# Performance work log

Hardware: AMD Instinct MI355X
Metric: run time of the kernel (lower is better)

Reference implementation:

```python
import jax, jax.numpy as jnp
import numpy as np

LN_EPS = 1e-5

def setup_inputs() -> dict:
    key = jax.random.key(0)
    k0, k1, k2, k3 = jax.random.split(key, 4)
    B, N, D = 4, 4096, 512
    x = jax.random.normal(k0, (B, N, D), dtype=jnp.float32)
    s = 1.0 / np.sqrt(D)
    Wq = jax.random.normal(k1, (D, D), dtype=jnp.float32) * s
    Wk = jax.random.normal(k2, (D, D), dtype=jnp.float32) * s
    Wv = jax.random.normal(k3, (D, D), dtype=jnp.float32) * s
    gamma = jnp.ones((D,), dtype=jnp.float32)
    beta = jnp.zeros((D,), dtype=jnp.float32)
    return {"x": x, "Wq": Wq, "Wk": Wk, "Wv": Wv, "gamma": gamma, "beta": beta}

def reference(x, Wq, Wk, Wv, gamma, beta):
    # x: [B, N, D]
    D = x.shape[-1]
    q = jnp.einsum('bnd,de->bne', x, Wq)
    k = jnp.einsum('bnd,de->bne', x, Wk)
    v = jnp.einsum('bnd,de->bne', x, Wv)
    # full [B, N, N] score matrix, as in the original bmm chain
    dist = jnp.einsum('bne,bme->bnm', q, k) * (1.0 / jnp.sqrt(jnp.float32(D)))
    dist = jax.nn.softmax(dist, axis=-1)
    att = jnp.einsum('bnm,bmd->bnd', dist, v)
    # residual + LayerNorm over last dim
    h = att + x
    mu = jnp.mean(h, axis=-1, keepdims=True)
    var = jnp.mean(jnp.square(h - mu), axis=-1, keepdims=True)
    out = (h - mu) * jax.lax.rsqrt(var + LN_EPS) * gamma + beta
    return out
```

## Files before the change

### kernel.cpp

```cpp
#include <hip/hip_runtime.h>
#include <stdint.h>

typedef __attribute__((ext_vector_type(8))) __bf16 bf16x8;
typedef __attribute__((ext_vector_type(4))) float f32x4;
typedef __attribute__((ext_vector_type(16))) float f32x16;
typedef unsigned short u16;
typedef unsigned char u8;
typedef unsigned int u32;
typedef long i64;

#define LN_EPS 1e-5f

__device__ __forceinline__ float bf2f(u16 u){
  union { u32 i; float f; } v; v.i = ((u32)u) << 16; return v.f;
}
__device__ __forceinline__ u16 f2bf(float f){
  union { float f; u32 i; } v; v.f = f;
  u32 u = v.i;
  u += 0x7fffu + ((u >> 16) & 1u);
  return (u16)(u >> 16);
}
__device__ __forceinline__ u8 f2fp8(float f){
  union { float f; u32 i; } v; v.f = f;
  u32 s = (v.i >> 24) & 0x80u;
  u32 u = v.i & 0x7FFFFFFFu;
  if (u < 0x3C800000u) return (u8)s;
  if (u > 0x43E00000u) u = 0x43E00000u;
  u += 0x7FFFFu + ((u >> 20) & 1u);
  int e = (int)(u >> 23) - 120;
  u32 m = (u >> 20) & 7u;
  return (u8)(s | ((u32)e << 3) | m);
}

__device__ __forceinline__ void gload_lds16(const void* g, void* l) {
  __builtin_amdgcn_global_load_lds(
      (const __attribute__((address_space(1))) void*)g,
      (__attribute__((address_space(3))) void*)l, 16, 0, 0);
}

__global__ void transpose_w_kernel(const float* __restrict__ Wq,
                                   const float* __restrict__ Wk,
                                   const float* __restrict__ Wv,
                                   u16* __restrict__ Wt) {
  const float* W = (blockIdx.y == 0) ? Wq : ((blockIdx.y == 1) ? Wk : Wv);
  u16* o = Wt + blockIdx.y * 512 * 512;
  int idx = blockIdx.x * 256 + threadIdx.x;
  int e = idx >> 9, d = idx & 511;
  o[e * 512 + d] = f2bf(W[d * 512 + e]);
}

__launch_bounds__(256, 2)
__global__ void qkv_gemm_kernel(const float* __restrict__ X,
                                const u16* __restrict__ Wt,
                                u8* __restrict__ Qo,
                                u8* __restrict__ Ko,
                                u16* __restrict__ Vto) {
  const int z = blockIdx.y;
  const u16* Wtm = Wt + z * 512 * 512;
  const int mblk = blockIdx.x & 127;
  const int nblk = blockIdx.x >> 7;
  const int m0 = mblk * 128, n0 = nblk * 128;

  __shared__ u16 As[128 * 40];
  __shared__ u16 Bs[128 * 40];

  const int tid = threadIdx.x;
  const int lane = tid & 63, w = tid >> 6;
  const int wr = w >> 1, wc = w & 1;
  const int lrow = lane & 15, quad = lane >> 4;

  f32x4 acc[4][4];
#pragma unroll
  for (int i = 0; i < 4; i++)
#pragma unroll
    for (int j = 0; j < 4; j++) acc[i][j] = (f32x4){0.f, 0.f, 0.f, 0.f};

  for (int k0 = 0; k0 < 512; k0 += 32) {
    __syncthreads();
#pragma unroll
    for (int i = 0; i < 2; i++) {
      int c = tid + i * 256;
      int r = c >> 2, cc = (c & 3) * 8;
      float4 f0 = *(const float4*)&X[(m0 + r) * 512 + k0 + cc];
      float4 f1 = *(const float4*)&X[(m0 + r) * 512 + k0 + cc + 4];
      ushort4 lo, hi;
      lo.x = f2bf(f0.x); lo.y = f2bf(f0.y); lo.z = f2bf(f0.z); lo.w = f2bf(f0.w);
      hi.x = f2bf(f1.x); hi.y = f2bf(f1.y); hi.z = f2bf(f1.z); hi.w = f2bf(f1.w);
      *(ushort4*)&As[r * 40 + cc] = lo;
      *(ushort4*)&As[r * 40 + cc + 4] = hi;
      uint4 vb = *(const uint4*)&Wtm[(n0 + r) * 512 + k0 + cc];
      *(uint4*)&Bs[r * 40 + cc] = vb;
    }
    __syncthreads();
    bf16x8 a[4], b[4];
#pragma unroll
    for (int t = 0; t < 4; t++)
      a[t] = *(const bf16x8*)&As[(wr * 64 + t * 16 + lrow) * 40 + quad * 8];
#pragma unroll
    for (int t = 0; t < 4; t++)
      b[t] = *(const bf16x8*)&Bs[(wc * 64 + t * 16 + lrow) * 40 + quad * 8];
#pragma unroll
    for (int i = 0; i < 4; i++)
#pragma unroll
      for (int j = 0; j < 4; j++)
        acc[i][j] = __builtin_amdgcn_mfma_f32_16x16x32_bf16(a[i], b[j], acc[i][j], 0, 0, 0);
  }

  if (z < 2) {
    u8* O = (z == 0) ? Qo : Ko;
#pragma unroll
    for (int i = 0; i < 4; i++) {
      int rbase = m0 + wr * 64 + i * 16 + quad * 4;
#pragma unroll
      for (int j = 0; j < 4; j++) {
        int col = n0 + wc * 64 + j * 16 + lrow;
#pragma unroll
        for (int r = 0; r < 4; r++)
          O[(rbase + r) * 512 + col] = f2fp8(acc[i][j][r]);
      }
    }
  } else {
#pragma unroll
    for (int i = 0; i < 4; i++) {
      int rbase = m0 + wr * 64 + i * 16 + quad * 4;
#pragma unroll
      for (int j = 0; j < 4; j++) {
        int col = n0 + wc * 64 + j * 16 + lrow;
        ushort4 pk;
        pk.x = f2bf(acc[i][j][0]);
        pk.y = f2bf(acc[i][j][1]);
        pk.z = f2bf(acc[i][j][2]);
        pk.w = f2bf(acc[i][j][3]);
        *(ushort4*)&Vto[col * 16384 + rbase] = pk;
      }
    }
  }
}

__launch_bounds__(256, 2)
__global__ void attn_partial_kernel(const u8* __restrict__ Q,
                                    const u8* __restrict__ K,
                                    const u16* __restrict__ Vt,
                                    float* __restrict__ O0,
                                    u16* __restrict__ O1,
                                    float* __restrict__ L) {
  const int b = blockIdx.y;
  const int split = blockIdx.z;
  const int q0 = blockIdx.x * 64;
  const int tid = threadIdx.x;
  const int lane = tid & 63, w = tid >> 6;
  const int lrow = lane & 15, quad = lane >> 4;
  const int l31 = lane & 31, half = lane >> 5;

  __shared__ __align__(16) u8 Ks8[32 * 512];
  __shared__ u16 Vs[512 * 32];
  __shared__ u16 Pbuf[64 * 40];

  const int keybase = b * 4096 + split * 2048;

  const int qtok = b * 4096 + q0 + w * 16 + lrow;
  i64 qf[16];
#pragma unroll
  for (int s = 0; s < 16; s++)
    qf[s] = *(const i64*)&Q[qtok * 512 + s * 32 + quad * 8];

  f32x16 Oacc[2][4];
#pragma unroll
  for (int i = 0; i < 2; i++)
#pragma unroll
    for (int j = 0; j < 4; j++)
#pragma unroll
      for (int e = 0; e < 16; e++) Oacc[i][j][e] = 0.f;

  float lsum[4] = {0.f, 0.f, 0.f, 0.f};
  const float scale = 0.044194173824159216f;

#pragma unroll
  for (int i = 0; i < 4; i++) {
    int row = w * 8 + i * 2 + (lane >> 5);
    int g = (lane & 31) ^ (row & 7);
    gload_lds16(&K[(keybase + row) * 512 + g * 16], &Ks8[(w * 8 + i * 2) * 512]);
  }
#pragma unroll
  for (int run = 0; run < 8; run++) {
    int rr = w * 8 + run;
    int n = rr * 16 + (lane >> 2);
    int c = (lane & 3) ^ (n & 3) ^ ((n >> 2) & 3);
    gload_lds16(&Vt[n * 16384 + keybase + c * 8], &Vs[rr * 512]);
  }

  for (int it = 0; it < 64; ++it) {
    __syncthreads();

    f32x4 S0 = {0.f, 0.f, 0.f, 0.f}, S1 = {0.f, 0.f, 0.f, 0.f};
#pragma unroll
    for (int s = 0; s < 16; s++) {
      int gs = (2 * s + (quad >> 1)) ^ (lrow & 7);
      int off = gs * 16 + (quad & 1) * 8;
      i64 k0 = *(const i64*)&Ks8[lrow * 512 + off];
      i64 k1 = *(const i64*)&Ks8[(16 + lrow) * 512 + off];
      S0 = __builtin_amdgcn_mfma_f32_16x16x32_fp8_fp8(qf[s], k0, S0, 0, 0, 0);
      S1 = __builtin_amdgcn_mfma_f32_16x16x32_fp8_fp8(qf[s], k1, S1, 0, 0, 0);
    }

#pragma unroll
    for (int r = 0; r < 4; r++) {
      float p0 = __expf(S0[r] * scale);
      float p1 = __expf(S1[r] * scale);
      lsum[r] += p0 + p1;
      int prow = w * 16 + quad * 4 + r;
      Pbuf[prow * 40 + lrow] = f2bf(p0);
      Pbuf[prow * 40 + 16 + lrow] = f2bf(p1);
    }

    __syncthreads();

    const int kknext = (it + 1) * 32;
    if (it < 63) {
#pragma unroll
      for (int i = 0; i < 4; i++) {
        int row = w * 8 + i * 2 + (lane >> 5);
        int g = (lane & 31) ^ (row & 7);
        gload_lds16(&K[(keybase + kknext + row) * 512 + g * 16],
                    &Ks8[(w * 8 + i * 2) * 512]);
      }
    }

    bf16x8 af[2][2];
#pragma unroll
    for (int i = 0; i < 2; i++)
#pragma unroll
      for (int kg = 0; kg < 2; kg++)
        af[i][kg] = *(const bf16x8*)&Pbuf[(i * 32 + l31) * 40 + kg * 16 + half * 8];

    bf16x8 bv[4][2];
#pragma unroll
    for (int j = 0; j < 4; j++)
#pragma unroll
      for (int kg = 0; kg < 2; kg++) {
        int n = w * 128 + j * 32 + l31;
        int c = (kg * 2 + half) ^ (n & 3) ^ ((n >> 2) & 3);
        bv[j][kg] = *(const bf16x8*)&Vs[n * 32 + c * 8];
      }

    asm volatile("s_waitcnt lgkmcnt(0)" ::: "memory");

    if (it < 63) {
#pragma unroll
      for (int run = 0; run < 8; run++) {
        int rr = w * 8 + run;
        int n = rr * 16 + (lane >> 2);
        int c = (lane & 3) ^ (n & 3) ^ ((n >> 2) & 3);
        gload_lds16(&Vt[n * 16384 + keybase + kknext + c * 8], &Vs[rr * 512]);
      }
    }

#pragma unroll
    for (int j = 0; j < 4; j++)
#pragma unroll
      for (int i = 0; i < 2; i++) {
        Oacc[i][j] = __builtin_amdgcn_mfma_f32_32x32x16_bf16(af[i][0], bv[j][0], Oacc[i][j], 0, 0, 0);
        Oacc[i][j] = __builtin_amdgcn_mfma_f32_32x32x16_bf16(af[i][1], bv[j][1], Oacc[i][j], 0, 0, 0);
      }
  }

#pragma unroll
  for (int r = 0; r < 4; r++) {
    float s = lsum[r];
    s += __shfl_xor(s, 1); s += __shfl_xor(s, 2);
    s += __shfl_xor(s, 4); s += __shfl_xor(s, 8);
    lsum[r] = s;
  }
  const int tokw = b * 4096 + q0 + w * 16 + quad * 4;
  if (lrow == 0) {
#pragma unroll
    for (int r = 0; r < 4; r++)
      L[split * 16384 + tokw + r] = lsum[r];
  }

  const int tokbase = b * 4096 + q0;
  if (split == 0) {
#pragma unroll
    for (int i = 0; i < 2; i++)
#pragma unroll
      for (int j = 0; j < 4; j++) {
        int col = w * 128 + j * 32 + l31;
#pragma unroll
        for (int p = 0; p < 16; p++) {
          int row = i * 32 + (p & 3) + 8 * (p >> 2) + 4 * half;
          O0[(tokbase + row) * 512 + col] = Oacc[i][j][p];
        }
      }
  } else {
#pragma unroll
    for (int i = 0; i < 2; i++)
#pragma unroll
      for (int j = 0; j < 4; j++) {
        int col = w * 128 + j * 32 + l31;
#pragma unroll
        for (int p = 0; p < 16; p++) {
          int row = i * 32 + (p & 3) + 8 * (p >> 2) + 4 * half;
          O1[(tokbase + row) * 512 + col] = f2bf(Oacc[i][j][p]);
        }
      }
  }
}

__launch_bounds__(256)
__global__ void combine_ln_kernel(const float* __restrict__ O0in,
                                  const u16* __restrict__ O1,
                                  const float* __restrict__ L,
                                  const float* __restrict__ X,
                                  const float* __restrict__ gamma,
                                  const float* __restrict__ beta,
                                  float* __restrict__ Out) {
  const int lane = threadIdx.x & 63;
  const int tok = blockIdx.x * 4 + (threadIdx.x >> 6);
  const float inv_l = 1.f / (L[tok] + L[16384 + tok]);
  const int base = tok * 512 + lane * 8;

  float4 a0 = *(const float4*)&O0in[base];
  float4 a1 = *(const float4*)&O0in[base + 4];
  uint4 bvec = *(const uint4*)&O1[base];
  const u16* bp = (const u16*)&bvec;
  float4 x0 = *(const float4*)&X[base];
  float4 x1 = *(const float4*)&X[base + 4];

  float h[8];
  h[0] = (a0.x + bf2f(bp[0])) * inv_l + x0.x;
  h[1] = (a0.y + bf2f(bp[1])) * inv_l + x0.y;
  h[2] = (a0.z + bf2f(bp[2])) * inv_l + x0.z;
  h[3] = (a0.w + bf2f(bp[3])) * inv_l + x0.w;
  h[4] = (a1.x + bf2f(bp[4])) * inv_l + x1.x;
  h[5] = (a1.y + bf2f(bp[5])) * inv_l + x1.y;
  h[6] = (a1.z + bf2f(bp[6])) * inv_l + x1.z;
  h[7] = (a1.w + bf2f(bp[7])) * inv_l + x1.w;

  float sum = 0.f, sq = 0.f;
#pragma unroll
  for (int i = 0; i < 8; i++) { sum += h[i]; sq += h[i] * h[i]; }
#pragma unroll
  for (int d = 1; d < 64; d <<= 1) {
    sum += __shfl_xor(sum, d);
    sq  += __shfl_xor(sq, d);
  }
  float mu = sum * (1.f / 512.f);
  float var = sq * (1.f / 512.f) - mu * mu;
  float rstd = rsqrtf(var + LN_EPS);

  float4 g0 = *(const float4*)&gamma[lane * 8];
  float4 g1 = *(const float4*)&gamma[lane * 8 + 4];
  float4 b0 = *(const float4*)&beta[lane * 8];
  float4 b1 = *(const float4*)&beta[lane * 8 + 4];

  float4 o0, o1;
  o0.x = (h[0] - mu) * rstd * g0.x + b0.x;
  o0.y = (h[1] - mu) * rstd * g0.y + b0.y;
  o0.z = (h[2] - mu) * rstd * g0.z + b0.z;
  o0.w = (h[3] - mu) * rstd * g0.w + b0.w;
  o1.x = (h[4] - mu) * rstd * g1.x + b1.x;
  o1.y = (h[5] - mu) * rstd * g1.y + b1.y;
  o1.z = (h[6] - mu) * rstd * g1.z + b1.z;
  o1.w = (h[7] - mu) * rstd * g1.w + b1.w;
  *(float4*)&Out[base] = o0;
  *(float4*)&Out[base + 4] = o1;
}

extern "C" void kernel_launch(void* const* d_in, const int* in_sizes, int n_in,
                              void* d_out, int out_size, void* d_ws, size_t ws_size,
                              hipStream_t stream) {
  const float* x = (const float*)d_in[0];
  const float* Wq = (const float*)d_in[1];
  const float* Wk = (const float*)d_in[2];
  const float* Wv = (const float*)d_in[3];
  const float* gamma = (const float*)d_in[4];
  const float* beta = (const float*)d_in[5];

  char* ws = (char*)d_ws;
  u8*  Qws   = (u8*)(ws);
  u8*  Kws   = (u8*)(ws + 8388608);
  u16* Vtws  = (u16*)(ws + 16777216);
  u16* Wtws  = (u16*)(ws + 33554432);
  u16* O1ws  = (u16*)(ws + 35127296);
  float* Lws = (float*)(ws + 51904512);
  float* O0  = (float*)d_out;

  hipLaunchKernelGGL(transpose_w_kernel, dim3(1024, 3), dim3(256), 0, stream,
                     Wq, Wk, Wv, Wtws);
  hipLaunchKernelGGL(qkv_gemm_kernel, dim3(512, 3), dim3(256), 0, stream,
                     x, Wtws, Qws, Kws, Vtws);
  hipLaunchKernelGGL(attn_partial_kernel, dim3(64, 4, 2), dim3(256), 0, stream,
                     Qws, Kws, Vtws, O0, O1ws, Lws);
  hipLaunchKernelGGL(combine_ln_kernel, dim3(4096), dim3(256), 0, stream,
                     O0, O1ws, Lws, x, gamma, beta, (float*)d_out);
}
```

Measured before the change: 290.8 us.

## Switch PV to fp8 MFMA, pre-cast X to bf16, async-load GEMM tiles

The attention PV product now uses fp8 probabilities and an fp8 transposed V with 32x32x16 fp8 MFMAs, which halves V staging bytes and LDS traffic. X is cast to bf16 in a separate kernel so the QKV GEMM can load tiles straight into swizzled LDS with global_load_lds, and the GEMM now asks for higher occupancy. Both partial attention outputs are stored as bf16 rather than one in fp32, which cuts write and read traffic in the combine step. The cost is lower precision in P and V, which could hurt accuracy, plus an extra launch and a reuse of the Xb workspace as O0b.

Measured after the change: 282.9 us. 1.03x faster.

```diff
diff --git a/kernel.cpp b/kernel.cpp
--- a/kernel.cpp
+++ b/kernel.cpp
@@ -38,6 +38,17 @@
       (__attribute__((address_space(3))) void*)l, 16, 0, 0);
 }
 
+__global__ void xcast_kernel(const float* __restrict__ X, u16* __restrict__ Xb) {
+  int idx = (blockIdx.x * 256 + threadIdx.x) * 8;
+  float4 f0 = *(const float4*)&X[idx];
+  float4 f1 = *(const float4*)&X[idx + 4];
+  ushort4 lo, hi;
+  lo.x = f2bf(f0.x); lo.y = f2bf(f0.y); lo.z = f2bf(f0.z); lo.w = f2bf(f0.w);
+  hi.x = f2bf(f1.x); hi.y = f2bf(f1.y); hi.z = f2bf(f1.z); hi.w = f2bf(f1.w);
+  *(ushort4*)&Xb[idx] = lo;
+  *(ushort4*)&Xb[idx + 4] = hi;
+}
+
 __global__ void transpose_w_kernel(const float* __restrict__ Wq,
                                    const float* __restrict__ Wk,
                                    const float* __restrict__ Wv,
@@ -49,20 +60,20 @@
   o[e * 512 + d] = f2bf(W[d * 512 + e]);
 }
 
-__launch_bounds__(256, 2)
-__global__ void qkv_gemm_kernel(const float* __restrict__ X,
+__launch_bounds__(256, 4)
+__global__ void qkv_gemm_kernel(const u16* __restrict__ Xb,
                                 const u16* __restrict__ Wt,
                                 u8* __restrict__ Qo,
                                 u8* __restrict__ Ko,
-                                u16* __restrict__ Vto) {
+                                u8* __restrict__ Vto8) {
   const int z = blockIdx.y;
   const u16* Wtm = Wt + z * 512 * 512;
   const int mblk = blockIdx.x & 127;
   const int nblk = blockIdx.x >> 7;
   const int m0 = mblk * 128, n0 = nblk * 128;
 
-  __shared__ u16 As[128 * 40];
-  __shared__ u16 Bs[128 * 40];
+  __shared__ __align__(16) u8 As[128 * 64];
+  __shared__ __align__(16) u8 Bs[128 * 64];
 
   const int tid = threadIdx.x;
   const int lane = tid & 63, w = tid >> 6;
@@ -75,30 +86,40 @@
 #pragma unroll
     for (int j = 0; j < 4; j++) acc[i][j] = (f32x4){0.f, 0.f, 0.f, 0.f};
 
-  for (int k0 = 0; k0 < 512; k0 += 32) {
-    __syncthreads();
-#pragma unroll
-    for (int i = 0; i < 2; i++) {
-      int c = tid + i * 256;
-      int r = c >> 2, cc = (c & 3) * 8;
-      float4 f0 = *(const float4*)&X[(m0 + r) * 512 + k0 + cc];
-      float4 f1 = *(const float4*)&X[(m0 + r) * 512 + k0 + cc + 4];
-      ushort4 lo, hi;
-      lo.x = f2bf(f0.x); lo.y = f2bf(f0.y); lo.z = f2bf(f0.z); lo.w = f2bf(f0.w);
-      hi.x = f2bf(f1.x); hi.y = f2bf(f1.y); hi.z = f2bf(f1.z); hi.w = f2bf(f1.w);
-      *(ushort4*)&As[r * 40 + cc] = lo;
-      *(ushort4*)&As[r * 40 + cc + 4] = hi;
-      uint4 vb = *(const uint4*)&Wtm[(n0 + r) * 512 + k0 + cc];
-      *(uint4*)&Bs[r * 40 + cc] = vb;
-    }
+  const int srow = lane >> 2;
+  const int spos = lane & 3;
+
+#pragma unroll
+  for (int r2 = 0; r2 < 2; r2++) {
+    int rowb = w * 32 + r2 * 16;
+    int row = rowb + srow;
+    int g = spos ^ (row & 3);
+    gload_lds16(&Xb[(m0 + row) * 512 + g * 8], &As[rowb * 64]);
+    gload_lds16(&Wtm[(n0 + row) * 512 + g * 8], &Bs[rowb * 64]);
+  }
+
+  for (int k = 0; k < 16; k++) {
     __syncthreads();
     bf16x8 a[4], b[4];
 #pragma unroll
-    for (int t = 0; t < 4; t++)
-      a[t] = *(const bf16x8*)&As[(wr * 64 + t * 16 + lrow) * 40 + quad * 8];
-#pragma unroll
-    for (int t = 0; t < 4; t++)
-      b[t] = *(const bf16x8*)&Bs[(wc * 64 + t * 16 + lrow) * 40 + quad * 8];
+    for (int t = 0; t < 4; t++) {
+      int ra = wr * 64 + t * 16 + lrow;
+      a[t] = *(const bf16x8*)&As[ra * 64 + (quad ^ (ra & 3)) * 16];
+      int rb = wc * 64 + t * 16 + lrow;
+      b[t] = *(const bf16x8*)&Bs[rb * 64 + (quad ^ (rb & 3)) * 16];
+    }
+    __syncthreads();
+    if (k < 15) {
+      int k0n = (k + 1) * 32;
+#pragma unroll
+      for (int r2 = 0; r2 < 2; r2++) {
+        int rowb = w * 32 + r2 * 16;
+        int row = rowb + srow;
+        int g = spos ^ (row & 3);
+        gload_lds16(&Xb[(m0 + row) * 512 + k0n + g * 8], &As[rowb * 64]);
+        gload_lds16(&Wtm[(n0 + row) * 512 + k0n + g * 8], &Bs[rowb * 64]);
+      }
+    }
 #pragma unroll
     for (int i = 0; i < 4; i++)
 #pragma unroll
@@ -126,12 +147,12 @@
 #pragma unroll
       for (int j = 0; j < 4; j++) {
         int col = n0 + wc * 64 + j * 16 + lrow;
-        ushort4 pk;
-        pk.x = f2bf(acc[i][j][0]);
-        pk.y = f2bf(acc[i][j][1]);
-        pk.z = f2bf(acc[i][j][2]);
-        pk.w = f2bf(acc[i][j][3]);
-        *(ushort4*)&Vto[col * 16384 + rbase] = pk;
+        uchar4 pk;
+        pk.x = f2fp8(acc[i][j][0]);
+        pk.y = f2fp8(acc[i][j][1]);
+        pk.z = f2fp8(acc[i][j][2]);
+        pk.w = f2fp8(acc[i][j][3]);
+        *(uchar4*)&Vto8[col * 16384 + rbase] = pk;
       }
     }
   }
@@ -140,9 +161,9 @@
 __launch_bounds__(256, 2)
 __global__ void attn_partial_kernel(const u8* __restrict__ Q,
                                     const u8* __restrict__ K,
-                                    const u16* __restrict__ Vt,
-                                    float* __restrict__ O0,
-                                    u16* __restrict__ O1,
+                                    const u8* __restrict__ Vt8,
+                                    u16* __restrict__ O0b,
+                                    u16* __restrict__ O1b,
                                     float* __restrict__ L) {
   const int b = blockIdx.y;
   const int split = blockIdx.z;
@@ -153,8 +174,8 @@
   const int l31 = lane & 31, half = lane >> 5;
 
   __shared__ __align__(16) u8 Ks8[32 * 512];
-  __shared__ u16 Vs[512 * 32];
-  __shared__ u16 Pbuf[64 * 40];
+  __shared__ __align__(16) u8 Vs8[512 * 32];
+  __shared__ __align__(16) u8 Pb8[64 * 40];
 
   const int keybase = b * 4096 + split * 2048;
 
@@ -182,11 +203,11 @@
     gload_lds16(&K[(keybase + row) * 512 + g * 16], &Ks8[(w * 8 + i * 2) * 512]);
   }
 #pragma unroll
-  for (int run = 0; run < 8; run++) {
-    int rr = w * 8 + run;
-    int n = rr * 16 + (lane >> 2);
-    int c = (lane & 3) ^ (n & 3) ^ ((n >> 2) & 3);
-    gload_lds16(&Vt[n * 16384 + keybase + c * 8], &Vs[rr * 512]);
+  for (int run = 0; run < 4; run++) {
+    int rowb = w * 128 + run * 32;
+    int n = rowb + (lane >> 1);
+    int g16 = (lane & 1) ^ ((n >> 2) & 1);
+    gload_lds16(&Vt8[n * 16384 + keybase + g16 * 16], &Vs8[rowb * 32]);
   }
 
   for (int it = 0; it < 64; ++it) {
@@ -209,8 +230,8 @@
       float p1 = __expf(S1[r] * scale);
       lsum[r] += p0 + p1;
       int prow = w * 16 + quad * 4 + r;
-      Pbuf[prow * 40 + lrow] = f2bf(p0);
-      Pbuf[prow * 40 + 16 + lrow] = f2bf(p1);
+      Pb8[prow * 40 + lrow] = f2fp8(p0);
+      Pb8[prow * 40 + 16 + lrow] = f2fp8(p1);
     }
 
     __syncthreads();
@@ -226,41 +247,41 @@
       }
     }
 
-    bf16x8 af[2][2];
+    i64 af[2][2];
 #pragma unroll
     for (int i = 0; i < 2; i++)
 #pragma unroll
       for (int kg = 0; kg < 2; kg++)
-        af[i][kg] = *(const bf16x8*)&Pbuf[(i * 32 + l31) * 40 + kg * 16 + half * 8];
-
-    bf16x8 bv[4][2];
+        af[i][kg] = *(const i64*)&Pb8[(i * 32 + l31) * 40 + kg * 16 + half * 8];
+
+    i64 bv[4][2];
+#pragma unroll
+    for (int j = 0; j < 4; j++) {
+      int n = w * 128 + j * 32 + l31;
+      int x = (n >> 2) & 1;
+#pragma unroll
+      for (int kg = 0; kg < 2; kg++)
+        bv[j][kg] = *(const i64*)&Vs8[n * 32 + (kg ^ x) * 16 + half * 8];
+    }
+
+    asm volatile("s_waitcnt lgkmcnt(0)" ::: "memory");
+
+    if (it < 63) {
+#pragma unroll
+      for (int run = 0; run < 4; run++) {
+        int rowb = w * 128 + run * 32;
+        int n = rowb + (lane >> 1);
+        int g16 = (lane & 1) ^ ((n >> 2) & 1);
+        gload_lds16(&Vt8[n * 16384 + keybase + kknext + g16 * 16], &Vs8[rowb * 32]);
+      }
+    }
+
 #pragma unroll
     for (int j = 0; j < 4; j++)
 #pragma unroll
-      for (int kg = 0; kg < 2; kg++) {
-        int n = w * 128 + j * 32 + l31;
-        int c = (kg * 2 + half) ^ (n & 3) ^ ((n >> 2) & 3);
-        bv[j][kg] = *(const bf16x8*)&Vs[n * 32 + c * 8];
-      }
-
-    asm volatile("s_waitcnt lgkmcnt(0)" ::: "memory");
-
-    if (it < 63) {
-#pragma unroll
-      for (int run = 0; run < 8; run++) {
-        int rr = w * 8 + run;
-        int n = rr * 16 + (lane >> 2);
-        int c = (lane & 3) ^ (n & 3) ^ ((n >> 2) & 3);
-        gload_lds16(&Vt[n * 16384 + keybase + kknext + c * 8], &Vs[rr * 512]);
-      }
-    }
-
-#pragma unroll
-    for (int j = 0; j < 4; j++)
-#pragma unroll
       for (int i = 0; i < 2; i++) {
-        Oacc[i][j] = __builtin_amdgcn_mfma_f32_32x32x16_bf16(af[i][0], bv[j][0], Oacc[i][j], 0, 0, 0);
-        Oacc[i][j] = __builtin_amdgcn_mfma_f32_32x32x16_bf16(af[i][1], bv[j][1], Oacc[i][j], 0, 0, 0);
+        Oacc[i][j] = __builtin_amdgcn_mfma_f32_32x32x16_fp8_fp8(af[i][0], bv[j][0], Oacc[i][j], 0, 0, 0);
+        Oacc[i][j] = __builtin_amdgcn_mfma_f32_32x32x16_fp8_fp8(af[i][1], bv[j][1], Oacc[i][j], 0, 0, 0);
       }
   }
 
@@ -278,37 +299,24 @@
       L[split * 16384 + tokw + r] = lsum[r];
   }
 
+  u16* Ob = (split == 0) ? O0b : O1b;
   const int tokbase = b * 4096 + q0;
-  if (split == 0) {
-#pragma unroll
-    for (int i = 0; i < 2; i++)
-#pragma unroll
-      for (int j = 0; j < 4; j++) {
-        int col = w * 128 + j * 32 + l31;
-#pragma unroll
-        for (int p = 0; p < 16; p++) {
-          int row = i * 32 + (p & 3) + 8 * (p >> 2) + 4 * half;
-          O0[(tokbase + row) * 512 + col] = Oacc[i][j][p];
-        }
-      }
-  } else {
-#pragma unroll
-    for (int i = 0; i < 2; i++)
-#pragma unroll
-      for (int j = 0; j < 4; j++) {
-        int col = w * 128 + j * 32 + l31;
-#pragma unroll
-        for (int p = 0; p < 16; p++) {
-          int row = i * 32 + (p & 3) + 8 * (p >> 2) + 4 * half;
-          O1[(tokbase + row) * 512 + col] = f2bf(Oacc[i][j][p]);
-        }
-      }
-  }
+#pragma unroll
+  for (int i = 0; i < 2; i++)
+#pragma unroll
+    for (int j = 0; j < 4; j++) {
+      int col = w * 128 + j * 32 + l31;
+#pragma unroll
+      for (int p = 0; p < 16; p++) {
+        int row = i * 32 + (p & 3) + 8 * (p >> 2) + 4 * half;
+        Ob[(tokbase + row) * 512 + col] = f2bf(Oacc[i][j][p]);
+      }
+    }
 }
 
 __launch_bounds__(256)
-__global__ void combine_ln_kernel(const float* __restrict__ O0in,
-                                  const u16* __restrict__ O1,
+__global__ void combine_ln_kernel(const u16* __restrict__ O0b,
+                                  const u16* __restrict__ O1b,
                                   const float* __restrict__ L,
                                   const float* __restrict__ X,
                                   const float* __restrict__ gamma,
@@ -319,22 +327,20 @@
   const float inv_l = 1.f / (L[tok] + L[16384 + tok]);
   const int base = tok * 512 + lane * 8;
 
-  float4 a0 = *(const float4*)&O0in[base];
-  float4 a1 = *(const float4*)&O0in[base + 4];
-  uint4 bvec = *(const uint4*)&O1[base];
+  uint4 avec = *(const uint4*)&O0b[base];
+  uint4 bvec = *(const uint4*)&O1b[base];
+  const u16* ap = (const u16*)&avec;
   const u16* bp = (const u16*)&bvec;
   float4 x0 = *(const float4*)&X[base];
   float4 x1 = *(const float4*)&X[base + 4];
+  const float* xp = (const float*)&x0;
+  float xs[8] = {x0.x, x0.y, x0.z, x0.w, x1.x, x1.y, x1.z, x1.w};
+  (void)xp;
 
   float h[8];
-  h[0] = (a0.x + bf2f(bp[0])) * inv_l + x0.x;
-  h[1] = (a0.y + bf2f(bp[1])) * inv_l + x0.y;
-  h[2] = (a0.z + bf2f(bp[2])) * inv_l + x0.z;
-  h[3] = (a0.w + bf2f(bp[3])) * inv_l + x0.w;
-  h[4] = (a1.x + bf2f(bp[4])) * inv_l + x1.x;
-  h[5] = (a1.y + bf2f(bp[5])) * inv_l + x1.y;
-  h[6] = (a1.z + bf2f(bp[6])) * inv_l + x1.z;
-  h[7] = (a1.w + bf2f(bp[7])) * inv_l + x1.w;
+#pragma unroll
+  for (int i = 0; i < 8; i++)
+    h[i] = (bf2f(ap[i]) + bf2f(bp[i])) * inv_l + xs[i];
 
   float sum = 0.f, sq = 0.f;
 #pragma unroll
@@ -352,16 +358,16 @@
   float4 g1 = *(const float4*)&gamma[lane * 8 + 4];
   float4 b0 = *(const float4*)&beta[lane * 8];
   float4 b1 = *(const float4*)&beta[lane * 8 + 4];
+  float gs[8] = {g0.x, g0.y, g0.z, g0.w, g1.x, g1.y, g1.z, g1.w};
+  float bs[8] = {b0.x, b0.y, b0.z, b0.w, b1.x, b1.y, b1.z, b1.w};
 
   float4 o0, o1;
-  o0.x = (h[0] - mu) * rstd * g0.x + b0.x;
-  o0.y = (h[1] - mu) * rstd * g0.y + b0.y;
-  o0.z = (h[2] - mu) * rstd * g0.z + b0.z;
-  o0.w = (h[3] - mu) * rstd * g0.w + b0.w;
-  o1.x = (h[4] - mu) * rstd * g1.x + b1.x;
-  o1.y = (h[5] - mu) * rstd * g1.y + b1.y;
-  o1.z = (h[6] - mu) * rstd * g1.z + b1.z;
-  o1.w = (h[7] - mu) * rstd * g1.w + b1.w;
+  float* op = (float*)&o0;
+#pragma unroll
+  for (int i = 0; i < 4; i++) op[i] = (h[i] - mu) * rstd * gs[i] + bs[i];
+  float* op1 = (float*)&o1;
+#pragma unroll
+  for (int i = 0; i < 4; i++) op1[i] = (h[i + 4] - mu) * rstd * gs[i + 4] + bs[i + 4];
   *(float4*)&Out[base] = o0;
   *(float4*)&Out[base + 4] = o1;
 }
@@ -379,18 +385,20 @@
   char* ws = (char*)d_ws;
   u8*  Qws   = (u8*)(ws);
   u8*  Kws   = (u8*)(ws + 8388608);
-  u16* Vtws  = (u16*)(ws + 16777216);
-  u16* Wtws  = (u16*)(ws + 33554432);
-  u16* O1ws  = (u16*)(ws + 35127296);
-  float* Lws = (float*)(ws + 51904512);
-  float* O0  = (float*)d_out;
-
+  u8*  Vt8ws = (u8*)(ws + 16777216);
+  u16* Wtws  = (u16*)(ws + 25165824);
+  u16* Xbws  = (u16*)(ws + 26738688);
+  u16* O0bws = (u16*)(ws + 26738688);
+  u16* O1bws = (u16*)(ws + 43515904);
+  float* Lws = (float*)(ws + 60293120);
+
+  hipLaunchKernelGGL(xcast_kernel, dim3(4096), dim3(256), 0, stream, x, Xbws);
   hipLaunchKernelGGL(transpose_w_kernel, dim3(1024, 3), dim3(256), 0, stream,
                      Wq, Wk, Wv, Wtws);
   hipLaunchKernelGGL(qkv_gemm_kernel, dim3(512, 3), dim3(256), 0, stream,
-                     x, Wtws, Qws, Kws, Vtws);
+                     Xbws, Wtws, Qws, Kws, Vt8ws);
   hipLaunchKernelGGL(attn_partial_kernel, dim3(64, 4, 2), dim3(256), 0, stream,
-                     Qws, Kws, Vtws, O0, O1ws, Lws);
+                     Qws, Kws, Vt8ws, O0bws, O1bws, Lws);
   hipLaunchKernelGGL(combine_ln_kernel, dim3(4096), dim3(256), 0, stream,
-                     O0, O1ws, Lws, x, gamma, beta, (float*)d_out);
-}
+                     O0bws, O1bws, Lws, x, gamma, beta, (float*)d_out);
+}
```
